# Kernel tuning notes

Hardware: AMD Instinct MI355X
Metric: run time of the kernel (lower is better)

Reference implementation:

```python
import jax, jax.numpy as jnp
import numpy as np

DIM = 512
HIDDEN = 2048
BATCH = 16384
NUM_VECTORS = 3


def _mlp(z, W1, b1, W2, b2, W3, b3):
    # 3-layer tanh MLP: dim -> hidden -> hidden -> dim
    h = jnp.tanh(z @ W1.T + b1)
    h = jnp.tanh(h @ W2.T + b2)
    return h @ W3.T + b3


def setup_inputs() -> dict:
    key = jax.random.key(0)
    ks = jax.random.split(key, 10)
    t = jnp.zeros((1,), dtype=jnp.float32)
    augmented_state = jax.random.normal(ks[0], (BATCH, DIM + 1), dtype=jnp.float32)
    epsilons = jax.random.normal(ks[1], (NUM_VECTORS, BATCH, DIM), dtype=jnp.float32)
    # Xavier-normal-ish init with gain 0.1 (final layer randomized instead of the
    # original zero-init so outputs/grads are non-trivial for kernel testing).
    def xavier(k, fan_out, fan_in, gain=0.1):
        std = gain * np.sqrt(2.0 / (fan_in + fan_out))
        return (jax.random.normal(k, (fan_out, fan_in), dtype=jnp.float32) * std)
    W1 = xavier(ks[2], HIDDEN, DIM)
    b1 = jnp.zeros((HIDDEN,), dtype=jnp.float32)
    W2 = xavier(ks[3], HIDDEN, HIDDEN)
    b2 = jnp.zeros((HIDDEN,), dtype=jnp.float32)
    W3 = xavier(ks[4], DIM, HIDDEN)
    b3 = jnp.zeros((DIM,), dtype=jnp.float32)
    return {"t": t, "augmented_state": augmented_state, "epsilons": epsilons,
            "W1": W1, "b1": b1, "W2": W2, "b2": b2, "W3": W3, "b3": b3}


def reference(t, augmented_state, epsilons, W1, b1, W2, b2, W3, b3):
    dim = W1.shape[1]
    z = augmented_state[:, :dim]                      # [B, dim]
    dz_dt = _mlp(z, W1, b1, W2, b2, W3, b3)           # [B, dim]
    # torch code computes g = d(sum f(z))/dz = J^T @ 1 (same for every loop
    # iteration since only epsilon is resampled), then averages (g * eps).sum(1).
    g = jax.grad(lambda zz: _mlp(zz, W1, b1, W2, b2, W3, b3).sum())(z)  # [B, dim]
    num_vectors = epsilons.shape[0]
    trace = jnp.einsum('kbd,bd->b', epsilons, g)[:, None] / num_vectors  # [B, 1]
    return jnp.concatenate([dz_dt, trace], axis=1)    # [B, dim+1]
```

## Files before the change

### kernel.cpp

```cpp
#include <hip/hip_runtime.h>
#include <hip/hip_bf16.h>
#include <stdint.h>

#define DIM 512
#define HIDDEN 2048
#define BATCH 16384

using bf16 = __hip_bfloat16;
typedef float f32x4 __attribute__((ext_vector_type(4)));
typedef short bf16x8 __attribute__((ext_vector_type(8)));

__device__ __forceinline__ float bf2f(bf16 x) { return __bfloat162float(x); }
__device__ __forceinline__ bf16 f2bf(float x) { return __float2bfloat16(x); }

__device__ __forceinline__ float fast_tanh(float x) {
    float e = __expf(2.0f * x);
    return 1.0f - 2.0f * __builtin_amdgcn_rcpf(e + 1.0f);
}

__device__ __forceinline__ f32x4 mfma16(bf16x8 a, bf16x8 b, f32x4 c) {
    return __builtin_amdgcn_mfma_f32_16x16x32_bf16(a, b, c, 0, 0, 0);
}

__device__ __forceinline__ void BARP() {
    __builtin_amdgcn_sched_barrier(0);
    __builtin_amdgcn_s_barrier();
    __builtin_amdgcn_sched_barrier(0);
}
__device__ __forceinline__ void LGK0_SB() {
    asm volatile("s_waitcnt lgkmcnt(0)" ::: "memory");
    __builtin_amdgcn_sched_barrier(0);
}
__device__ __forceinline__ void VMC4() {
    asm volatile("s_waitcnt vmcnt(4)" ::: "memory");
}

__device__ __forceinline__ void stage_half(const bf16* __restrict__ G, int grow0,
                                           int Kdim, int kbase, bf16* lds,
                                           int elem_base, int wave, int srow4, int gs8)
{
#pragma unroll
    for (int i = 0; i < 2; ++i) {
        const int q = wave * 2 + i;
        const bf16* ga = G + (size_t)(grow0 + q * 16 + srow4) * Kdim + kbase + gs8;
        __builtin_amdgcn_global_load_lds(
            (const __attribute__((address_space(1))) void*)ga,
            (__attribute__((address_space(3))) void*)(lds + elem_base + q * 512), 16, 0, 0);
    }
}

template <int MODE>
__global__ __launch_bounds__(512, 2)
void gemm8(const bf16* __restrict__ A, const bf16* __restrict__ Bt,
           int M, int N, int K,
           const float* __restrict__ bias,
           bf16* __restrict__ out1, bf16* __restrict__ out2,
           const float* __restrict__ u3, const bf16* __restrict__ h1s)
{
    __shared__ bf16 lds[65536];
    const int tid  = threadIdx.x;
    const int lane = tid & 63;
    const int wave = tid >> 6;

    const int nwg = gridDim.x * gridDim.y;
    const int bid = blockIdx.y * gridDim.x + blockIdx.x;
    const int cpx = nwg >> 3;
    const int sw  = (bid & 7) * cpx + (bid >> 3);
    const int nbn = N >> 8;
    const int bm  = sw / nbn;
    const int bn  = sw % nbn;
    const int row0 = bm << 8;
    const int col0 = bn << 8;

    const int wr = wave >> 2;
    const int wc = wave & 3;
    const int l15 = lane & 15;

    const int slotl    = (((lane >> 4) ^ (l15 & 3)) << 4);
    const int laneoffA = (wr * 128 + l15) * 64 + slotl;
    const int laneoffB = (wc * 64  + l15) * 64 + slotl;
    const int srow4 = lane >> 2;
    const int gs8   = (((lane & 3) ^ ((lane >> 2) & 3)) << 3);

    const char* ldsc = (const char*)lds;
    f32x4 acc[8][4] = {};
    bf16x8 af[8];

    stage_half(A,  row0, K, 0,  lds, 0,     wave, srow4, gs8);
    stage_half(Bt, col0, K, 0,  lds, 16384, wave, srow4, gs8);
    stage_half(A,  row0, K, 32, lds, 8192,  wave, srow4, gs8);
    stage_half(Bt, col0, K, 32, lds, 24576, wave, srow4, gs8);
    VMC4(); BARP();

    const int KT = K >> 6;
    for (int t = 0; t < KT; ++t) {
        const int cur = t & 1;
        const int cb  = cur << 16;
        const int ce  = (cur ^ 1) << 15;
        const int knt = ((t + 1 < KT) ? t + 1 : 0) << 6;

#pragma unroll
        for (int m = 0; m < 8; ++m)
            af[m] = *(const bf16x8*)(ldsc + cb + m * 1024 + laneoffA);
        bf16x8 b0 = *(const bf16x8*)(ldsc + cb + 32768 + laneoffB);
        bf16x8 b1 = *(const bf16x8*)(ldsc + cb + 32768 + 1024 + laneoffB);
        stage_half(A, row0, K, knt, lds, ce, wave, srow4, gs8);
        BARP(); LGK0_SB();
        __builtin_amdgcn_s_setprio(1);
#pragma unroll
        for (int m = 0; m < 8; ++m) {
            acc[m][0] = mfma16(af[m], b0, acc[m][0]);
            acc[m][1] = mfma16(af[m], b1, acc[m][1]);
        }
        __builtin_amdgcn_s_setprio(0);
        BARP();

        b0 = *(const bf16x8*)(ldsc + cb + 32768 + 2048 + laneoffB);
        b1 = *(const bf16x8*)(ldsc + cb + 32768 + 3072 + laneoffB);
        stage_half(Bt, col0, K, knt, lds, ce + 16384, wave, srow4, gs8);
        BARP(); LGK0_SB();
        __builtin_amdgcn_s_setprio(1);
#pragma unroll
        for (int m = 0; m < 8; ++m) {
            acc[m][2] = mfma16(af[m], b0, acc[m][2]);
            acc[m][3] = mfma16(af[m], b1, acc[m][3]);
        }
        __builtin_amdgcn_s_setprio(0);
        VMC4();
        BARP();

#pragma unroll
        for (int m = 0; m < 8; ++m)
            af[m] = *(const bf16x8*)(ldsc + cb + 16384 + m * 1024 + laneoffA);
        b0 = *(const bf16x8*)(ldsc + cb + 49152 + laneoffB);
        b1 = *(const bf16x8*)(ldsc + cb + 49152 + 1024 + laneoffB);
        stage_half(A, row0, K, knt + 32, lds, ce + 8192, wave, srow4, gs8);
        BARP(); LGK0_SB();
        __builtin_amdgcn_s_setprio(1);
#pragma unroll
        for (int m = 0; m < 8; ++m) {
            acc[m][0] = mfma16(af[m], b0, acc[m][0]);
            acc[m][1] = mfma16(af[m], b1, acc[m][1]);
        }
        __builtin_amdgcn_s_setprio(0);
        BARP();

        b0 = *(const bf16x8*)(ldsc + cb + 49152 + 2048 + laneoffB);
        b1 = *(const bf16x8*)(ldsc + cb + 49152 + 3072 + laneoffB);
        stage_half(Bt, col0, K, knt + 32, lds, ce + 24576, wave, srow4, gs8);
        BARP(); LGK0_SB();
        __builtin_amdgcn_s_setprio(1);
#pragma unroll
        for (int m = 0; m < 8; ++m) {
            acc[m][2] = mfma16(af[m], b0, acc[m][2]);
            acc[m][3] = mfma16(af[m], b1, acc[m][3]);
        }
        __builtin_amdgcn_s_setprio(0);
        VMC4();
        BARP();
    }

    const int c4 = (lane >> 4) << 2;
#pragma unroll
    for (int m = 0; m < 8; ++m) {
        const int growb = row0 + wr * 128 + m * 16 + c4;
#pragma unroll
        for (int n = 0; n < 4; ++n) {
            const int gcol = col0 + wc * 64 + n * 16 + l15;
            const float bz = (MODE == 3) ? 0.0f : bias[gcol];
            const float uu = (MODE == 1) ? u3[gcol] : 0.0f;
#pragma unroll
            for (int r = 0; r < 4; ++r) {
                const size_t idx = (size_t)(growb + r) * N + gcol;
                const float cv = acc[m][n][r];
                if (MODE == 0) {
                    out1[idx] = f2bf(fast_tanh(cv + bz));
                } else if (MODE == 1) {
                    float v = fast_tanh(cv + bz);
                    out1[idx] = f2bf(v);
                    out2[idx] = f2bf(uu * (1.0f - v * v));
                } else {
                    float h = bf2f(h1s[idx]);
                    out1[idx] = f2bf(cv * (1.0f - h * h));
                }
            }
        }
    }
}

template <int MODE>
__global__ __launch_bounds__(256)
void gemm_bt(const bf16* __restrict__ A, const bf16* __restrict__ Bt,
             int M, int N, int K,
             const float* __restrict__ bias,
             float* __restrict__ outF)
{
    __shared__ __align__(128) bf16 As[128 * 64];
    __shared__ __align__(128) bf16 Bs[128 * 64];

    const int tid  = threadIdx.x;
    const int lane = tid & 63;
    const int wave = tid >> 6;

    const int nwg = gridDim.x * gridDim.y;
    const int bid = blockIdx.y * gridDim.x + blockIdx.x;
    const int cpx = nwg >> 3;
    const int sw  = (bid & 7) * cpx + (bid >> 3);
    const int nbn = N >> 7;
    const int bm  = sw / nbn;
    const int bn  = sw % nbn;
    const int row0 = bm << 7;
    const int col0 = bn << 7;

    const int wr = wave >> 1;
    const int wc = wave & 1;

    f32x4 acc[4][4] = {};

    const int srow  = lane >> 3;
    const int sslot = lane & 7;

    const int KT = K >> 6;
    for (int kt = 0; kt < KT; ++kt) {
        const int k0 = kt << 6;
        __syncthreads();
#pragma unroll
        for (int i = 0; i < 4; ++i) {
            const int q   = wave * 4 + i;
            const int row = q * 8 + srow;
            const int gs  = sslot ^ (row & 7);
            const bf16* ga = A  + (size_t)(row0 + row) * K + (k0 + gs * 8);
            const bf16* gb = Bt + (size_t)(col0 + row) * K + (k0 + gs * 8);
            __builtin_amdgcn_global_load_lds(
                (const __attribute__((address_space(1))) void*)ga,
                (__attribute__((address_space(3))) void*)(As + q * 512), 16, 0, 0);
            __builtin_amdgcn_global_load_lds(
                (const __attribute__((address_space(1))) void*)gb,
                (__attribute__((address_space(3))) void*)(Bs + q * 512), 16, 0, 0);
        }
        __syncthreads();

#pragma unroll
        for (int half = 0; half < 2; ++half) {
            const int kb = half * 4 + (lane >> 4);
            bf16x8 af[4], bfr[4];
#pragma unroll
            for (int m = 0; m < 4; ++m) {
                const int ar = wr * 64 + m * 16 + (lane & 15);
                af[m] = *(const bf16x8*)((const char*)As + ar * 128 + ((kb ^ (ar & 7)) << 4));
            }
#pragma unroll
            for (int n = 0; n < 4; ++n) {
                const int br = wc * 64 + n * 16 + (lane & 15);
                bfr[n] = *(const bf16x8*)((const char*)Bs + br * 128 + ((kb ^ (br & 7)) << 4));
            }
#pragma unroll
            for (int m = 0; m < 4; ++m)
#pragma unroll
                for (int n = 0; n < 4; ++n)
                    acc[m][n] = mfma16(af[m], bfr[n], acc[m][n]);
        }
    }

    const int c_lo = lane & 15;
    const int c_hi = lane >> 4;
#pragma unroll
    for (int m = 0; m < 4; ++m) {
#pragma unroll
        for (int n = 0; n < 4; ++n) {
#pragma unroll
            for (int r = 0; r < 4; ++r) {
                const int grow = row0 + wr * 64 + m * 16 + c_hi * 4 + r;
                const int gcol = col0 + wc * 64 + n * 16 + c_lo;
                const float cv = acc[m][n][r];
                if (MODE == 2) {
                    outF[(size_t)grow * 513 + gcol] = cv + bias[gcol];
                } else {
                    outF[(size_t)grow * N + gcol] = cv;
                }
            }
        }
    }
}


__global__ void eps_reduce(const float* __restrict__ eps, float* __restrict__ esum, int n)
{
    const float4* e0 = (const float4*)eps;
    const float4* e1 = (const float4*)(eps + (size_t)n);
    const float4* e2 = (const float4*)(eps + 2 * (size_t)n);
    float4* o = (float4*)esum;
    const int n4 = n >> 2;
    const int stride = gridDim.x * blockDim.x;
    for (int i = blockIdx.x * blockDim.x + threadIdx.x; i < n4; i += stride) {
        float4 a = e0[i], b = e1[i], c = e2[i];
        o[i] = make_float4(a.x + b.x + c.x, a.y + b.y + c.y,
                           a.z + b.z + c.z, a.w + b.w + c.w);
    }
}

__global__ void z_convert(const float* __restrict__ aug, bf16* __restrict__ zb)
{
    const int stride = gridDim.x * blockDim.x;
    for (int i = blockIdx.x * blockDim.x + threadIdx.x; i < BATCH * DIM; i += stride) {
        const int b = i >> 9, d = i & 511;
        zb[i] = f2bf(aug[(size_t)b * 513 + d]);
    }
}

__global__ void conv_bf16(const float* __restrict__ src, bf16* __restrict__ dst, int n)
{
    const int stride = gridDim.x * blockDim.x;
    for (int i = blockIdx.x * blockDim.x + threadIdx.x; i < n; i += stride)
        dst[i] = f2bf(src[i]);
}

__global__ void transpose_bf16(const float* __restrict__ src, bf16* __restrict__ dst,
                               int R, int C)
{
    __shared__ float t[32][33];
    const int bx = blockIdx.x * 32;
    const int by = blockIdx.y * 32;
    const int tx = threadIdx.x & 31;
    const int ty = threadIdx.x >> 5;
#pragma unroll
    for (int j = 0; j < 32; j += 8)
        t[ty + j][tx] = src[(size_t)(by + ty + j) * C + (bx + tx)];
    __syncthreads();
#pragma unroll
    for (int j = 0; j < 32; j += 8)
        dst[(size_t)(bx + ty + j) * R + (by + tx)] = f2bf(t[tx][ty + j]);
}

__global__ void colsum(const float* __restrict__ W3, float* __restrict__ u3)
{
    const int j = blockIdx.x * blockDim.x + threadIdx.x;
    if (j >= HIDDEN) return;
    float s = 0.f;
    for (int i = 0; i < DIM; ++i) s += W3[(size_t)i * HIDDEN + j];
    u3[j] = s;
}

__global__ void trace_kernel(const float* __restrict__ esum, const float* __restrict__ g,
                             float* __restrict__ out)
{
    const int row  = blockIdx.x * 4 + (threadIdx.x >> 6);
    const int lane = threadIdx.x & 63;
    const float4* e  = (const float4*)(esum + (size_t)row * 512);
    const float4* gg = (const float4*)(g + (size_t)row * 512);
    float s = 0.f;
#pragma unroll
    for (int i = 0; i < 2; ++i) {
        float4 a = e[lane * 2 + i], b = gg[lane * 2 + i];
        s += a.x * b.x + a.y * b.y + a.z * b.z + a.w * b.w;
    }
#pragma unroll
    for (int off = 1; off < 64; off <<= 1) s += __shfl_xor(s, off);
    if (lane == 0) out[(size_t)row * 513 + 512] = s * (1.0f / 3.0f);
}

extern "C" void kernel_launch(void* const* d_in, const int* in_sizes, int n_in,
                              void* d_out, int out_size, void* d_ws, size_t ws_size,
                              hipStream_t stream)
{
    const float* aug = (const float*)d_in[1];
    const float* eps = (const float*)d_in[2];
    const float* W1  = (const float*)d_in[3];
    const float* b1  = (const float*)d_in[4];
    const float* W2  = (const float*)d_in[5];
    const float* b2  = (const float*)d_in[6];
    const float* W3  = (const float*)d_in[7];
    const float* b3  = (const float*)d_in[8];
    float* out = (float*)d_out;

    char* ws = (char*)d_ws;
    size_t off = 0;
    auto alloc = [&](size_t bytes) {
        char* p = ws + off;
        off += (bytes + 255) & ~(size_t)255;
        return p;
    };
    bf16*  zb   = (bf16*)alloc((size_t)BATCH * DIM * 2);
    bf16*  h1   = (bf16*)alloc((size_t)BATCH * HIDDEN * 2);
    bf16*  h2   = (bf16*)alloc((size_t)BATCH * HIDDEN * 2);
    bf16*  d2   = (bf16*)alloc((size_t)BATCH * HIDDEN * 2);
    float* g    = (float*)alloc((size_t)BATCH * DIM * 4);
    float* esum = (float*)alloc((size_t)BATCH * DIM * 4);
    bf16*  W1b  = (bf16*)alloc((size_t)HIDDEN * DIM * 2);
    bf16*  W2b  = (bf16*)alloc((size_t)HIDDEN * HIDDEN * 2);
    bf16*  W3b  = (bf16*)alloc((size_t)DIM * HIDDEN * 2);
    bf16*  W2t  = (bf16*)alloc((size_t)HIDDEN * HIDDEN * 2);
    bf16*  W1t  = (bf16*)alloc((size_t)DIM * HIDDEN * 2);
    float* u3   = (float*)alloc((size_t)HIDDEN * 4);
    bf16*  d1   = h2;

    eps_reduce<<<2048, 256, 0, stream>>>(eps, esum, BATCH * DIM);
    z_convert<<<2048, 256, 0, stream>>>(aug, zb);
    conv_bf16<<<1024, 256, 0, stream>>>(W1, W1b, HIDDEN * DIM);
    conv_bf16<<<2048, 256, 0, stream>>>(W2, W2b, HIDDEN * HIDDEN);
    conv_bf16<<<1024, 256, 0, stream>>>(W3, W3b, DIM * HIDDEN);
    transpose_bf16<<<dim3(HIDDEN / 32, HIDDEN / 32), 256, 0, stream>>>(W2, W2t, HIDDEN, HIDDEN);
    transpose_bf16<<<dim3(DIM / 32, HIDDEN / 32), 256, 0, stream>>>(W1, W1t, HIDDEN, DIM);
    colsum<<<HIDDEN / 256, 256, 0, stream>>>(W3, u3);

    dim3 g8(BATCH / 256, HIDDEN / 256);
    dim3 gSml(BATCH / 128, DIM / 128);
    gemm8<0><<<g8, 512, 0, stream>>>(zb, W1b, BATCH, HIDDEN, DIM, b1,
                                     h1, nullptr, nullptr, nullptr);
    gemm8<1><<<g8, 512, 0, stream>>>(h1, W2b, BATCH, HIDDEN, HIDDEN, b2,
                                     h2, d2, u3, nullptr);
    gemm_bt<2><<<gSml, 256, 0, stream>>>(h2, W3b, BATCH, DIM, HIDDEN, b3, out);
    gemm8<3><<<g8, 512, 0, stream>>>(d2, W2t, BATCH, HIDDEN, HIDDEN, nullptr,
                                     d1, nullptr, nullptr, h1);
    gemm_bt<4><<<gSml, 256, 0, stream>>>(d1, W1t, BATCH, DIM, HIDDEN, nullptr, g);
    trace_kernel<<<BATCH / 4, 256, 0, stream>>>(esum, g, out);
}
```

Measured before the change: 687.5 us.

## Fuse trace reduction into last GEMM epilogue and retile gemm8 inner MFMA loop

The final input-gradient GEMM now multiplies its accumulators by the summed epsilons in its epilogue and reduces them with shuffles. It atomically adds the scaled trace into the output column, which removes the g buffer write, its re-read and the separate trace kernel. The trace column is zeroed in z_convert, which runs earlier in the launch sequence. Separately, the 256x256 gemm8 inner loop is reorganised into 4x4 MFMA blocks that reload A fragments per half instead of holding all eight, and its LDS swizzle pattern is changed. The reorder trades fewer live fragment registers for more LDS reads, and the atomics add contention on the trace column.

```diff
diff --git a/kernel.cpp b/kernel.cpp
--- a/kernel.cpp
+++ b/kernel.cpp
@@ -76,15 +76,15 @@
     const int wc = wave & 3;
     const int l15 = lane & 15;
 
-    const int slotl    = (((lane >> 4) ^ (l15 & 3)) << 4);
+    const int slotl    = (((lane >> 4) ^ ((l15 >> 1) & 3)) << 4);
     const int laneoffA = (wr * 128 + l15) * 64 + slotl;
     const int laneoffB = (wc * 64  + l15) * 64 + slotl;
     const int srow4 = lane >> 2;
-    const int gs8   = (((lane & 3) ^ ((lane >> 2) & 3)) << 3);
+    const int gs8   = (((lane & 3) ^ ((lane >> 3) & 3)) << 3);
 
     const char* ldsc = (const char*)lds;
     f32x4 acc[8][4] = {};
-    bf16x8 af[8];
+    bf16x8 af[4], bfv[4];
 
     stage_half(A,  row0, K, 0,  lds, 0,     wave, srow4, gs8);
     stage_half(Bt, col0, K, 0,  lds, 16384, wave, srow4, gs8);
@@ -100,61 +100,65 @@
         const int knt = ((t + 1 < KT) ? t + 1 : 0) << 6;
 
 #pragma unroll
-        for (int m = 0; m < 8; ++m)
-            af[m] = *(const bf16x8*)(ldsc + cb + m * 1024 + laneoffA);
-        bf16x8 b0 = *(const bf16x8*)(ldsc + cb + 32768 + laneoffB);
-        bf16x8 b1 = *(const bf16x8*)(ldsc + cb + 32768 + 1024 + laneoffB);
+        for (int j = 0; j < 4; ++j)
+            af[j] = *(const bf16x8*)(ldsc + cb + j * 1024 + laneoffA);
+#pragma unroll
+        for (int j = 0; j < 4; ++j)
+            bfv[j] = *(const bf16x8*)(ldsc + cb + 32768 + j * 1024 + laneoffB);
         stage_half(A, row0, K, knt, lds, ce, wave, srow4, gs8);
         BARP(); LGK0_SB();
         __builtin_amdgcn_s_setprio(1);
 #pragma unroll
-        for (int m = 0; m < 8; ++m) {
-            acc[m][0] = mfma16(af[m], b0, acc[m][0]);
-            acc[m][1] = mfma16(af[m], b1, acc[m][1]);
-        }
+        for (int m = 0; m < 4; ++m)
+#pragma unroll
+            for (int n = 0; n < 4; ++n)
+                acc[m][n] = mfma16(af[m], bfv[n], acc[m][n]);
         __builtin_amdgcn_s_setprio(0);
         BARP();
 
-        b0 = *(const bf16x8*)(ldsc + cb + 32768 + 2048 + laneoffB);
-        b1 = *(const bf16x8*)(ldsc + cb + 32768 + 3072 + laneoffB);
+#pragma unroll
+        for (int j = 0; j < 4; ++j)
+            af[j] = *(const bf16x8*)(ldsc + cb + (4 + j) * 1024 + laneoffA);
         stage_half(Bt, col0, K, knt, lds, ce + 16384, wave, srow4, gs8);
         BARP(); LGK0_SB();
         __builtin_amdgcn_s_setprio(1);
 #pragma unroll
-        for (int m = 0; m < 8; ++m) {
-            acc[m][2] = mfma16(af[m], b0, acc[m][2]);
-            acc[m][3] = mfma16(af[m], b1, acc[m][3]);
-        }
+        for (int m = 0; m < 4; ++m)
+#pragma unroll
+            for (int n = 0; n < 4; ++n)
+                acc[4 + m][n] = mfma16(af[m], bfv[n], acc[4 + m][n]);
         __builtin_amdgcn_s_setprio(0);
         VMC4();
         BARP();
 
 #pragma unroll
-        for (int m = 0; m < 8; ++m)
-            af[m] = *(const bf16x8*)(ldsc + cb + 16384 + m * 1024 + laneoffA);
-        b0 = *(const bf16x8*)(ldsc + cb + 49152 + laneoffB);
-        b1 = *(const bf16x8*)(ldsc + cb + 49152 + 1024 + laneoffB);
+        for (int j = 0; j < 4; ++j)
+            af[j] = *(const bf16x8*)(ldsc + cb + 16384 + j * 1024 + laneoffA);
+#pragma unroll
+        for (int j = 0; j < 4; ++j)
+            bfv[j] = *(const bf16x8*)(ldsc + cb + 49152 + j * 1024 + laneoffB);
         stage_half(A, row0, K, knt + 32, lds, ce + 8192, wave, srow4, gs8);
         BARP(); LGK0_SB();
         __builtin_amdgcn_s_setprio(1);
 #pragma unroll
-        for (int m = 0; m < 8; ++m) {
-            acc[m][0] = mfma16(af[m], b0, acc[m][0]);
-            acc[m][1] = mfma16(af[m], b1, acc[m][1]);
-        }
+        for (int m = 0; m < 4; ++m)
+#pragma unroll
+            for (int n = 0; n < 4; ++n)
+                acc[m][n] = mfma16(af[m], bfv[n], acc[m][n]);
         __builtin_amdgcn_s_setprio(0);
         BARP();
 
-        b0 = *(const bf16x8*)(ldsc + cb + 49152 + 2048 + laneoffB);
-        b1 = *(const bf16x8*)(ldsc + cb + 49152 + 3072 + laneoffB);
+#pragma unroll
+        for (int j = 0; j < 4; ++j)
+            af[j] = *(const bf16x8*)(ldsc + cb + 16384 + (4 + j) * 1024 + laneoffA);
         stage_half(Bt, col0, K, knt + 32, lds, ce + 24576, wave, srow4, gs8);
         BARP(); LGK0_SB();
         __builtin_amdgcn_s_setprio(1);
 #pragma unroll
-        for (int m = 0; m < 8; ++m) {
-            acc[m][2] = mfma16(af[m], b0, acc[m][2]);
-            acc[m][3] = mfma16(af[m], b1, acc[m][3]);
-        }
+        for (int m = 0; m < 4; ++m)
+#pragma unroll
+            for (int n = 0; n < 4; ++n)
+                acc[4 + m][n] = mfma16(af[m], bfv[n], acc[4 + m][n]);
         __builtin_amdgcn_s_setprio(0);
         VMC4();
         BARP();
@@ -193,7 +197,8 @@
 void gemm_bt(const bf16* __restrict__ A, const bf16* __restrict__ Bt,
              int M, int N, int K,
              const float* __restrict__ bias,
-             float* __restrict__ outF)
+             float* __restrict__ outF,
+             const float* __restrict__ esum)
 {
     __shared__ __align__(128) bf16 As[128 * 64];
     __shared__ __align__(128) bf16 Bs[128 * 64];
@@ -264,20 +269,35 @@
 
     const int c_lo = lane & 15;
     const int c_hi = lane >> 4;
-#pragma unroll
-    for (int m = 0; m < 4; ++m) {
-#pragma unroll
-        for (int n = 0; n < 4; ++n) {
+    if (MODE == 2) {
+#pragma unroll
+        for (int m = 0; m < 4; ++m)
+#pragma unroll
+            for (int n = 0; n < 4; ++n)
+#pragma unroll
+                for (int r = 0; r < 4; ++r) {
+                    const int grow = row0 + wr * 64 + m * 16 + c_hi * 4 + r;
+                    const int gcol = col0 + wc * 64 + n * 16 + c_lo;
+                    outF[(size_t)grow * 513 + gcol] = acc[m][n][r] + bias[gcol];
+                }
+    } else {
+#pragma unroll
+        for (int m = 0; m < 4; ++m) {
 #pragma unroll
             for (int r = 0; r < 4; ++r) {
                 const int grow = row0 + wr * 64 + m * 16 + c_hi * 4 + r;
-                const int gcol = col0 + wc * 64 + n * 16 + c_lo;
-                const float cv = acc[m][n][r];
-                if (MODE == 2) {
-                    outF[(size_t)grow * 513 + gcol] = cv + bias[gcol];
-                } else {
-                    outF[(size_t)grow * N + gcol] = cv;
+                float s = 0.f;
+#pragma unroll
+                for (int n = 0; n < 4; ++n) {
+                    const int gcol = col0 + wc * 64 + n * 16 + c_lo;
+                    s += acc[m][n][r] * esum[(size_t)grow * 512 + gcol];
                 }
+                s += __shfl_xor(s, 1);
+                s += __shfl_xor(s, 2);
+                s += __shfl_xor(s, 4);
+                s += __shfl_xor(s, 8);
+                if (c_lo == 0)
+                    atomicAdd(outF + (size_t)grow * 513 + 512, s * (1.0f / 3.0f));
             }
         }
     }
@@ -299,12 +319,14 @@
     }
 }
 
-__global__ void z_convert(const float* __restrict__ aug, bf16* __restrict__ zb)
+__global__ void z_convert(const float* __restrict__ aug, bf16* __restrict__ zb,
+                          float* __restrict__ out)
 {
     const int stride = gridDim.x * blockDim.x;
     for (int i = blockIdx.x * blockDim.x + threadIdx.x; i < BATCH * DIM; i += stride) {
         const int b = i >> 9, d = i & 511;
         zb[i] = f2bf(aug[(size_t)b * 513 + d]);
+        if (d == 0) out[(size_t)b * 513 + 512] = 0.f;
     }
 }
 
@@ -339,24 +361,6 @@
     float s = 0.f;
     for (int i = 0; i < DIM; ++i) s += W3[(size_t)i * HIDDEN + j];
     u3[j] = s;
-}
-
-__global__ void trace_kernel(const float* __restrict__ esum, const float* __restrict__ g,
-                             float* __restrict__ out)
-{
-    const int row  = blockIdx.x * 4 + (threadIdx.x >> 6);
-    const int lane = threadIdx.x & 63;
-    const float4* e  = (const float4*)(esum + (size_t)row * 512);
-    const float4* gg = (const float4*)(g + (size_t)row * 512);
-    float s = 0.f;
-#pragma unroll
-    for (int i = 0; i < 2; ++i) {
-        float4 a = e[lane * 2 + i], b = gg[lane * 2 + i];
-        s += a.x * b.x + a.y * b.y + a.z * b.z + a.w * b.w;
-    }
-#pragma unroll
-    for (int off = 1; off < 64; off <<= 1) s += __shfl_xor(s, off);
-    if (lane == 0) out[(size_t)row * 513 + 512] = s * (1.0f / 3.0f);
 }
 
 extern "C" void kernel_launch(void* const* d_in, const int* in_sizes, int n_in,
@@ -384,7 +388,6 @@
     bf16*  h1   = (bf16*)alloc((size_t)BATCH * HIDDEN * 2);
     bf16*  h2   = (bf16*)alloc((size_t)BATCH * HIDDEN * 2);
     bf16*  d2   = (bf16*)alloc((size_t)BATCH * HIDDEN * 2);
-    float* g    = (float*)alloc((size_t)BATCH * DIM * 4);
     float* esum = (float*)alloc((size_t)BATCH * DIM * 4);
     bf16*  W1b  = (bf16*)alloc((size_t)HIDDEN * DIM * 2);
     bf16*  W2b  = (bf16*)alloc((size_t)HIDDEN * HIDDEN * 2);
@@ -395,7 +398,7 @@
     bf16*  d1   = h2;
 
     eps_reduce<<<2048, 256, 0, stream>>>(eps, esum, BATCH * DIM);
-    z_convert<<<2048, 256, 0, stream>>>(aug, zb);
+    z_convert<<<2048, 256, 0, stream>>>(aug, zb, out);
     conv_bf16<<<1024, 256, 0, stream>>>(W1, W1b, HIDDEN * DIM);
     conv_bf16<<<2048, 256, 0, stream>>>(W2, W2b, HIDDEN * HIDDEN);
     conv_bf16<<<1024, 256, 0, stream>>>(W3, W3b, DIM * HIDDEN);
@@ -409,9 +412,8 @@
                                      h1, nullptr, nullptr, nullptr);
     gemm8<1><<<g8, 512, 0, stream>>>(h1, W2b, BATCH, HIDDEN, HIDDEN, b2,
                                      h2, d2, u3, nullptr);
-    gemm_bt<2><<<gSml, 256, 0, stream>>>(h2, W3b, BATCH, DIM, HIDDEN, b3, out);
+    gemm_bt<2><<<gSml, 256, 0, stream>>>(h2, W3b, BATCH, DIM, HIDDEN, b3, out, nullptr);
     gemm8<3><<<g8, 512, 0, stream>>>(d2, W2t, BATCH, HIDDEN, HIDDEN, nullptr,
                                      d1, nullptr, nullptr, h1);
-    gemm_bt<4><<<gSml, 256, 0, stream>>>(d1, W1t, BATCH, DIM, HIDDEN, nullptr, g);
-    trace_kernel<<<BATCH / 4, 256, 0, stream>>>(esum, g, out);
-}
+    gemm_bt<4><<<gSml, 256, 0, stream>>>(d1, W1t, BATCH, DIM, HIDDEN, nullptr, out, esum);
+}
```

After: 666.2 us. -3.1%, faster.
